# Kernel optimization log

Hardware: AMD Instinct MI355X
Metric: run time of the kernel (lower is better)

Reference implementation:

```python
import jax, jax.numpy as jnp
import numpy as np


def setup_inputs() -> dict:
    key = jax.random.key(0)
    k1, k2 = jax.random.split(key)
    B, G, P = 32, 64, 256
    pred_patches = jax.random.normal(k1, (B, G, P, 3), dtype=jnp.float32)
    target_patches = jax.random.normal(k2, (B, G, P, 3), dtype=jnp.float32)
    return {"pred_patches": pred_patches, "target_patches": target_patches}


def reference(pred_patches, target_patches):
    b, g, p, _ = pred_patches.shape
    pred = pred_patches.reshape(b * g, p, 3)    # (BG, P, 3)
    tgt = target_patches.reshape(b * g, p, 3)   # (BG, P, 3)
    # Squared euclidean distance via ||p||^2 + ||q||^2 - 2 p.q (matches cdist(p=2)**2)
    pn = jnp.sum(pred * pred, axis=-1)          # (BG, P)
    tn = jnp.sum(tgt * tgt, axis=-1)            # (BG, P)
    cross = jnp.einsum('bpd,bqd->bpq', pred, tgt)  # (BG, P, P)
    dist2 = jnp.maximum(pn[:, :, None] + tn[:, None, :] - 2.0 * cross, 0.0)
    forward_dist = jnp.min(dist2, axis=2).mean(axis=1)   # nearest target for each pred point
    backward_dist = jnp.min(dist2, axis=1).mean(axis=1)  # nearest pred for each target point
    per_patch = forward_dist + backward_dist             # (BG,)
    return jnp.mean(per_patch)  # reduction='mean' over batch*patches
```

## Files before the change

kernel.cpp:

```cpp
#include <hip/hip_runtime.h>


#define NPATCH 2048
#define NPTS   256

typedef float v2f __attribute__((ext_vector_type(2)));
typedef float v4f __attribute__((ext_vector_type(4)));

static __forceinline__ __device__ v2f splat2(float s) { return (v2f){s, s}; }
static __forceinline__ __device__ v2f fma2(v2f a, v2f b, v2f c) {
    return __builtin_elementwise_fma(a, b, c);
}
static __forceinline__ __device__ v2f min2(v2f a, v2f b) {
    return __builtin_elementwise_min(a, b);
}

__global__ __launch_bounds__(256, 4) void chamfer_patch_kernel(
    const float* __restrict__ pred,
    const float* __restrict__ tgt,
    float* __restrict__ partial)
{
    __shared__ float sP[3][NPTS];
    __shared__ float sT[3][NPTS];
    __shared__ float mhalf[2][NPTS];
    __shared__ float red[2];

    const int patch = blockIdx.x;
    const int tid   = threadIdx.x;

    {
        const float* __restrict__ pb = pred + (size_t)patch * (NPTS * 3);
        const float* __restrict__ tb = tgt  + (size_t)patch * (NPTS * 3);
        float x = pb[3 * tid + 0], y = pb[3 * tid + 1], z = pb[3 * tid + 2];
        sP[0][tid] = x; sP[1][tid] = y; sP[2][tid] = z;
        x = tb[3 * tid + 0]; y = tb[3 * tid + 1]; z = tb[3 * tid + 2];
        sT[0][tid] = x; sT[1][tid] = y; sT[2][tid] = z;
    }
    __syncthreads();

    const int wave = tid >> 6;
    const int lane = tid & 63;
    const int dir  = wave >> 1;
    const int half = wave & 1;

    const float (*Q)[NPTS] = (dir == 0) ? sP : sT;
    const float (*S)[NPTS] = (dir == 0) ? sT : sP;

    v2f qx2[4], qy2[4], qz2[4], m2[4];
    float qn[4];
#pragma unroll
    for (int q = 0; q < 4; ++q) {
        const int p = lane + 64 * q;
        const float x = Q[0][p], y = Q[1][p], z = Q[2][p];
        qx2[q] = splat2(-2.0f * x);
        qy2[q] = splat2(-2.0f * y);
        qz2[q] = splat2(-2.0f * z);
        qn[q]  = fmaf(z, z, fmaf(y, y, x * x));
        m2[q]  = (v2f){1e30f, 1e30f};
    }

    const int jbase = half * (NPTS / 2);
    const float* __restrict__ Sx = &S[0][jbase];
    const float* __restrict__ Sy = &S[1][jbase];
    const float* __restrict__ Sz = &S[2][jbase];

#pragma unroll 2
    for (int jj = 0; jj < NPTS / 2; jj += 4) {
        const v4f tx4 = *(const v4f*)(Sx + jj);
        const v4f ty4 = *(const v4f*)(Sy + jj);
        const v4f tz4 = *(const v4f*)(Sz + jj);

        {
            const v2f tx = {tx4.x, tx4.y}, ty = {ty4.x, ty4.y}, tz = {tz4.x, tz4.y};
            const v2f tn = fma2(tz, tz, fma2(ty, ty, tx * tx));
#pragma unroll
            for (int q = 0; q < 4; ++q) {
                v2f d = fma2(qx2[q], tx, tn);
                d = fma2(qy2[q], ty, d);
                d = fma2(qz2[q], tz, d);
                m2[q] = min2(m2[q], d);
            }
        }
        {
            const v2f tx = {tx4.z, tx4.w}, ty = {ty4.z, ty4.w}, tz = {tz4.z, tz4.w};
            const v2f tn = fma2(tz, tz, fma2(ty, ty, tx * tx));
#pragma unroll
            for (int q = 0; q < 4; ++q) {
                v2f d = fma2(qx2[q], tx, tn);
                d = fma2(qy2[q], ty, d);
                d = fma2(qz2[q], tz, d);
                m2[q] = min2(m2[q], d);
            }
        }
    }

    if (half == 1) {
#pragma unroll
        for (int q = 0; q < 4; ++q)
            mhalf[dir][lane + 64 * q] = fminf(m2[q].x, m2[q].y);
    }
    __syncthreads();

    if (half == 0) {
        float s = 0.0f;
#pragma unroll
        for (int q = 0; q < 4; ++q) {
            const float mm = fminf(fminf(m2[q].x, m2[q].y),
                                   mhalf[dir][lane + 64 * q]);
            s += fmaxf(qn[q] + mm, 0.0f);
        }
#pragma unroll
        for (int off = 32; off > 0; off >>= 1)
            s += __shfl_down(s, off, 64);
        if (lane == 0) red[dir] = s;
    }
    __syncthreads();
    if (tid == 0) partial[patch] = red[0] + red[1];
}

__global__ __launch_bounds__(256) void chamfer_reduce_kernel(
    const float* __restrict__ partial,
    float* __restrict__ out)
{
    __shared__ float red[4];
    const int tid = threadIdx.x;
    float s = 0.0f;
#pragma unroll
    for (int i = tid; i < NPATCH; i += 256) s += partial[i];
#pragma unroll
    for (int off = 32; off > 0; off >>= 1)
        s += __shfl_down(s, off, 64);
    if ((tid & 63) == 0) red[tid >> 6] = s;
    __syncthreads();
    if (tid == 0)
        out[0] = (red[0] + red[1] + red[2] + red[3]) *
                 (1.0f / ((float)NPTS * (float)NPATCH));
}

extern "C" void kernel_launch(void* const* d_in, const int* in_sizes, int n_in,
                              void* d_out, int out_size, void* d_ws, size_t ws_size,
                              hipStream_t stream) {
    const float* pred = (const float*)d_in[0];
    const float* tgt  = (const float*)d_in[1];
    float* partial    = (float*)d_ws;
    float* out        = (float*)d_out;

    chamfer_patch_kernel<<<NPATCH, 256, 0, stream>>>(pred, tgt, partial);
    chamfer_reduce_kernel<<<1, 256, 0, stream>>>(partial, out);
}
```

Measured before the change: 83.90 us.

## Precompute point norms, use scalar FMAs, fuse final reduction via atomics

Squared norms of every point are computed once at load time and stored in a fourth shared-memory row, so the inner loop no longer recomputes target norms. The packed v2f math is replaced with scalar fmaf chains and a deeper unroll. The separate reduce kernel is replaced by per-block atomic accumulation with a last-block counter, preceded by a memset of the workspace. This trades one launch for a memset plus 2048 global atomics, and summation order becomes nondeterministic.

```diff
diff --git a/kernel.cpp b/kernel.cpp
--- a/kernel.cpp
+++ b/kernel.cpp
@@ -4,24 +4,16 @@
 #define NPATCH 2048
 #define NPTS   256
 
-typedef float v2f __attribute__((ext_vector_type(2)));
 typedef float v4f __attribute__((ext_vector_type(4)));
 
-static __forceinline__ __device__ v2f splat2(float s) { return (v2f){s, s}; }
-static __forceinline__ __device__ v2f fma2(v2f a, v2f b, v2f c) {
-    return __builtin_elementwise_fma(a, b, c);
-}
-static __forceinline__ __device__ v2f min2(v2f a, v2f b) {
-    return __builtin_elementwise_min(a, b);
-}
-
-__global__ __launch_bounds__(256, 4) void chamfer_patch_kernel(
+__global__ __launch_bounds__(256, 4) void chamfer_kernel(
     const float* __restrict__ pred,
     const float* __restrict__ tgt,
-    float* __restrict__ partial)
+    float* __restrict__ ws,
+    float* __restrict__ out)
 {
-    __shared__ float sP[3][NPTS];
-    __shared__ float sT[3][NPTS];
+    __shared__ float sP[4][NPTS];
+    __shared__ float sT[4][NPTS];
     __shared__ float mhalf[2][NPTS];
     __shared__ float red[2];
 
@@ -33,8 +25,10 @@
         const float* __restrict__ tb = tgt  + (size_t)patch * (NPTS * 3);
         float x = pb[3 * tid + 0], y = pb[3 * tid + 1], z = pb[3 * tid + 2];
         sP[0][tid] = x; sP[1][tid] = y; sP[2][tid] = z;
+        sP[3][tid] = fmaf(z, z, fmaf(y, y, x * x));
         x = tb[3 * tid + 0]; y = tb[3 * tid + 1]; z = tb[3 * tid + 2];
         sT[0][tid] = x; sT[1][tid] = y; sT[2][tid] = z;
+        sT[3][tid] = fmaf(z, z, fmaf(y, y, x * x));
     }
     __syncthreads();
 
@@ -46,58 +40,44 @@
     const float (*Q)[NPTS] = (dir == 0) ? sP : sT;
     const float (*S)[NPTS] = (dir == 0) ? sT : sP;
 
-    v2f qx2[4], qy2[4], qz2[4], m2[4];
-    float qn[4];
+    float qx[4], qy[4], qz[4], qn[4], m[4];
 #pragma unroll
     for (int q = 0; q < 4; ++q) {
         const int p = lane + 64 * q;
-        const float x = Q[0][p], y = Q[1][p], z = Q[2][p];
-        qx2[q] = splat2(-2.0f * x);
-        qy2[q] = splat2(-2.0f * y);
-        qz2[q] = splat2(-2.0f * z);
-        qn[q]  = fmaf(z, z, fmaf(y, y, x * x));
-        m2[q]  = (v2f){1e30f, 1e30f};
+        qx[q] = -2.0f * Q[0][p];
+        qy[q] = -2.0f * Q[1][p];
+        qz[q] = -2.0f * Q[2][p];
+        qn[q] = Q[3][p];
+        m[q]  = 1e30f;
     }
 
     const int jbase = half * (NPTS / 2);
     const float* __restrict__ Sx = &S[0][jbase];
     const float* __restrict__ Sy = &S[1][jbase];
     const float* __restrict__ Sz = &S[2][jbase];
+    const float* __restrict__ Sn = &S[3][jbase];
 
-#pragma unroll 2
+#pragma unroll 8
     for (int jj = 0; jj < NPTS / 2; jj += 4) {
-        const v4f tx4 = *(const v4f*)(Sx + jj);
-        const v4f ty4 = *(const v4f*)(Sy + jj);
-        const v4f tz4 = *(const v4f*)(Sz + jj);
-
-        {
-            const v2f tx = {tx4.x, tx4.y}, ty = {ty4.x, ty4.y}, tz = {tz4.x, tz4.y};
-            const v2f tn = fma2(tz, tz, fma2(ty, ty, tx * tx));
+        const v4f x4 = *(const v4f*)(Sx + jj);
+        const v4f y4 = *(const v4f*)(Sy + jj);
+        const v4f z4 = *(const v4f*)(Sz + jj);
+        const v4f n4 = *(const v4f*)(Sn + jj);
 #pragma unroll
-            for (int q = 0; q < 4; ++q) {
-                v2f d = fma2(qx2[q], tx, tn);
-                d = fma2(qy2[q], ty, d);
-                d = fma2(qz2[q], tz, d);
-                m2[q] = min2(m2[q], d);
-            }
-        }
-        {
-            const v2f tx = {tx4.z, tx4.w}, ty = {ty4.z, ty4.w}, tz = {tz4.z, tz4.w};
-            const v2f tn = fma2(tz, tz, fma2(ty, ty, tx * tx));
-#pragma unroll
-            for (int q = 0; q < 4; ++q) {
-                v2f d = fma2(qx2[q], tx, tn);
-                d = fma2(qy2[q], ty, d);
-                d = fma2(qz2[q], tz, d);
-                m2[q] = min2(m2[q], d);
-            }
+        for (int q = 0; q < 4; ++q) {
+            const float da = fmaf(qx[q], x4.x, fmaf(qy[q], y4.x, fmaf(qz[q], z4.x, n4.x)));
+            const float db = fmaf(qx[q], x4.y, fmaf(qy[q], y4.y, fmaf(qz[q], z4.y, n4.y)));
+            m[q] = fminf(m[q], fminf(da, db));
+            const float dc = fmaf(qx[q], x4.z, fmaf(qy[q], y4.z, fmaf(qz[q], z4.z, n4.z)));
+            const float dd = fmaf(qx[q], x4.w, fmaf(qy[q], y4.w, fmaf(qz[q], z4.w, n4.w)));
+            m[q] = fminf(m[q], fminf(dc, dd));
         }
     }
 
     if (half == 1) {
 #pragma unroll
         for (int q = 0; q < 4; ++q)
-            mhalf[dir][lane + 64 * q] = fminf(m2[q].x, m2[q].y);
+            mhalf[dir][lane + 64 * q] = m[q];
     }
     __syncthreads();
 
@@ -105,8 +85,7 @@
         float s = 0.0f;
 #pragma unroll
         for (int q = 0; q < 4; ++q) {
-            const float mm = fminf(fminf(m2[q].x, m2[q].y),
-                                   mhalf[dir][lane + 64 * q]);
+            const float mm = fminf(m[q], mhalf[dir][lane + 64 * q]);
             s += fmaxf(qn[q] + mm, 0.0f);
         }
 #pragma unroll
@@ -115,26 +94,21 @@
         if (lane == 0) red[dir] = s;
     }
     __syncthreads();
-    if (tid == 0) partial[patch] = red[0] + red[1];
-}
 
-__global__ __launch_bounds__(256) void chamfer_reduce_kernel(
-    const float* __restrict__ partial,
-    float* __restrict__ out)
-{
-    __shared__ float red[4];
-    const int tid = threadIdx.x;
-    float s = 0.0f;
-#pragma unroll
-    for (int i = tid; i < NPATCH; i += 256) s += partial[i];
-#pragma unroll
-    for (int off = 32; off > 0; off >>= 1)
-        s += __shfl_down(s, off, 64);
-    if ((tid & 63) == 0) red[tid >> 6] = s;
-    __syncthreads();
-    if (tid == 0)
-        out[0] = (red[0] + red[1] + red[2] + red[3]) *
-                 (1.0f / ((float)NPTS * (float)NPATCH));
+    if (tid == 0) {
+        const float bsum = red[0] + red[1];
+        __hip_atomic_fetch_add(&ws[0], bsum, __ATOMIC_RELAXED,
+                               __HIP_MEMORY_SCOPE_AGENT);
+        __threadfence();
+        unsigned int* cnt = (unsigned int*)(ws + 1);
+        const unsigned int prev = __hip_atomic_fetch_add(
+            cnt, 1u, __ATOMIC_ACQ_REL, __HIP_MEMORY_SCOPE_AGENT);
+        if (prev == NPATCH - 1) {
+            const float total = __hip_atomic_load(&ws[0], __ATOMIC_ACQUIRE,
+                                                  __HIP_MEMORY_SCOPE_AGENT);
+            out[0] = total * (1.0f / ((float)NPTS * (float)NPATCH));
+        }
+    }
 }
 
 extern "C" void kernel_launch(void* const* d_in, const int* in_sizes, int n_in,
@@ -142,9 +116,9 @@
                               hipStream_t stream) {
     const float* pred = (const float*)d_in[0];
     const float* tgt  = (const float*)d_in[1];
-    float* partial    = (float*)d_ws;
+    float* ws         = (float*)d_ws;
     float* out        = (float*)d_out;
 
-    chamfer_patch_kernel<<<NPATCH, 256, 0, stream>>>(pred, tgt, partial);
-    chamfer_reduce_kernel<<<1, 256, 0, stream>>>(partial, out);
+    hipMemsetAsync(ws, 0, 8, stream);
+    chamfer_kernel<<<NPATCH, 256, 0, stream>>>(pred, tgt, ws, out);
 }
```

Result: slower. 138.5 us (+65.1%).
